# Optimization experiments

Hardware: AMD Instinct MI355X
Metric: run time of the kernel (lower is better)

The kernel has to match this reference:

```python
import jax, jax.numpy as jnp
import numpy as np
from jax import lax

B, H, W, C = 64, 224, 224, 3
FLAT = 27040  # 52*52*10 after localization convs/pools


def conv_relu(x, w, b):
    y = lax.conv_general_dilated(x, w, (1, 1), 'VALID',
                                 dimension_numbers=('NHWC', 'HWIO', 'NHWC'))
    return jax.nn.relu(y + b)


def maxpool2(x):
    return lax.reduce_window(x, -jnp.inf, lax.max, (1, 2, 2, 1), (1, 2, 2, 1), 'VALID')


def affine_grid(h, w, theta):
    # normalized coords in [-1, 1]
    xt, yt = jnp.meshgrid(jnp.linspace(-1.0, 1.0, w), jnp.linspace(-1.0, 1.0, h))
    grid = jnp.stack([xt.ravel(), yt.ravel(), jnp.ones(h * w, theta.dtype)], 0)  # (3, h*w)
    g = jnp.einsum('bij,jp->bip', theta, grid)  # (B, 2, h*w)
    return g.reshape(-1, 2, h, w)


def bilinear_sampler(img, xs, ys):
    # xs, ys: (B, h, w) in [-1, 1]; img: (B, H, W, C)
    max_y, max_x = img.shape[1] - 1, img.shape[2] - 1
    x = 0.5 * (xs + 1.0) * max_x
    y = 0.5 * (ys + 1.0) * max_y
    x0 = jnp.clip(jnp.floor(x).astype(jnp.int32), 0, max_x)
    x1 = jnp.clip(x0 + 1, 0, max_x)
    y0 = jnp.clip(jnp.floor(y).astype(jnp.int32), 0, max_y)
    y1 = jnp.clip(y0 + 1, 0, max_y)
    b = jnp.arange(img.shape[0])[:, None, None]
    Ia = img[b, y0, x0]  # (B,h,w,C)
    Ib = img[b, y1, x0]
    Ic = img[b, y0, x1]
    Id = img[b, y1, x1]
    x0f, x1f = x0.astype(x.dtype), x1.astype(x.dtype)
    y0f, y1f = y0.astype(y.dtype), y1.astype(y.dtype)
    wa = ((x1f - x) * (y1f - y))[..., None]
    wb = ((x1f - x) * (y - y0f))[..., None]
    wc = ((x - x0f) * (y1f - y))[..., None]
    wd = ((x - x0f) * (y - y0f))[..., None]
    return wa * Ia + wb * Ib + wc * Ic + wd * Id


def setup_inputs() -> dict:
    key = jax.random.key(0)
    ks = jax.random.split(key, 6)
    inputs = jax.random.normal(ks[0], (B, H, W, C), jnp.float32)
    conv1_w = jax.random.normal(ks[1], (7, 7, 3, 8), jnp.float32) * (2.0 / (7 * 7 * 3)) ** 0.5
    conv1_b = jnp.zeros((8,), jnp.float32)
    conv2_w = jax.random.normal(ks[2], (5, 5, 8, 10), jnp.float32) * (2.0 / (5 * 5 * 8)) ** 0.5
    conv2_b = jnp.zeros((10,), jnp.float32)
    fc1_w = jax.random.normal(ks[3], (FLAT, 32), jnp.float32) * (2.0 / FLAT) ** 0.5
    fc1_b = jnp.zeros((32,), jnp.float32)
    fc2_w = jax.random.normal(ks[4], (32, 6), jnp.float32) * 0.01
    fc2_b = jnp.array([1, 0, 0, 0, 1, 0], jnp.float32)  # identity affine init
    return dict(inputs=inputs, conv1_w=conv1_w, conv1_b=conv1_b,
                conv2_w=conv2_w, conv2_b=conv2_b, fc1_w=fc1_w, fc1_b=fc1_b,
                fc2_w=fc2_w, fc2_b=fc2_b)


def reference(inputs, conv1_w, conv1_b, conv2_w, conv2_b, fc1_w, fc1_b, fc2_w, fc2_b):
    xs = maxpool2(conv_relu(inputs, conv1_w, conv1_b))
    xs = maxpool2(conv_relu(xs, conv2_w, conv2_b))
    xs = xs.reshape(xs.shape[0], -1)  # (B, 27040)
    h1 = jax.nn.relu(xs @ fc1_w + fc1_b)
    theta = (h1 @ fc2_w + fc2_b).reshape(-1, 2, 3)
    grid = affine_grid(H, W, theta)  # (B, 2, H, W)
    return bilinear_sampler(inputs, grid[:, 0], grid[:, 1])
```

## Files before the change

kernel.cpp:

```cpp
#include <hip/hip_runtime.h>


__global__ __launch_bounds__(256) void k_wcvt(
    const float* __restrict__ w1, const float* __restrict__ b1,
    double* __restrict__ wd) {
  int t = blockIdx.x * 256 + threadIdx.x;
  if (t < 1176) wd[t] = (double)w1[t];
  else if (t < 1184) wd[t] = (double)b1[t - 1176];
}

__global__ __launch_bounds__(448) void k_conv1(
    const float* __restrict__ in, const double* __restrict__ wd,
    double* __restrict__ out) {
  __shared__ float win[14 * 672];

  int g = blockIdx.x & 7;
  int i = blockIdx.x >> 3;
  int b = g * 8 + i / 28;
  int tile = i % 28;
  int py0 = 4 * tile;
  int r0 = 8 * tile;

  {
    const float* ibb = in + (size_t)b * 150528;
    for (int idx = threadIdx.x; idx < 14 * 168; idx += 448) {
      int rr = idx / 168, c4 = idx % 168;
      int row = min(r0 + rr, 223);
      float4 v = reinterpret_cast<const float4*>(ibb + (size_t)row * 672)[c4];
      reinterpret_cast<float4*>(&win[rr * 672])[c4] = v;
    }
  }
  __syncthreads();

  int t = threadIdx.x;
  int py = py0 + t / 109;
  if (t < 436 && py < 109) {
    int px = t % 109;
    int lrb = 2 * (t / 109);

    double acc[2][2][8];
#pragma unroll
    for (int ii = 0; ii < 2; ++ii)
#pragma unroll
      for (int j = 0; j < 2; ++j)
#pragma unroll
        for (int k = 0; k < 8; ++k) acc[ii][j][k] = 0.0;

    for (int ky = 0; ky < 7; ++ky) {
      const float* r0p = &win[(lrb + ky) * 672 + 6 * px];
      const float* r1p = r0p + 672;
      float a0[24], a1[24];
#pragma unroll
      for (int j = 0; j < 12; ++j) {
        float2 u = reinterpret_cast<const float2*>(r0p)[j];
        a0[2 * j] = u.x; a0[2 * j + 1] = u.y;
        float2 v = reinterpret_cast<const float2*>(r1p)[j];
        a1[2 * j] = v.x; a1[2 * j + 1] = v.y;
      }
      const double* wk = wd + ky * 168;
#pragma unroll
      for (int kx = 0; kx < 7; ++kx) {
#pragma unroll
        for (int c = 0; c < 3; ++c) {
          double v00 = (double)a0[kx * 3 + c];
          double v01 = (double)a0[kx * 3 + 3 + c];
          double v10 = (double)a1[kx * 3 + c];
          double v11 = (double)a1[kx * 3 + 3 + c];
          const double* wp = wk + (kx * 3 + c) * 8;
#pragma unroll
          for (int oc = 0; oc < 8; ++oc) {
            double wv = wp[oc];
            acc[0][0][oc] = fma(v00, wv, acc[0][0][oc]);
            acc[0][1][oc] = fma(v01, wv, acc[0][1][oc]);
            acc[1][0][oc] = fma(v10, wv, acc[1][0][oc]);
            acc[1][1][oc] = fma(v11, wv, acc[1][1][oc]);
          }
        }
      }
    }

    double* op = out + ((size_t)b * 11881 + (size_t)py * 109 + px) * 8;
#pragma unroll
    for (int oc = 0; oc < 8; ++oc) {
      double m = fmax(fmax(acc[0][0][oc], acc[0][1][oc]),
                      fmax(acc[1][0][oc], acc[1][1][oc]));
      op[oc] = fmax(m + wd[1176 + oc], 0.0);
    }
  }
}

__global__ __launch_bounds__(448) void k_conv2(
    const double* __restrict__ in, const float* __restrict__ w,
    const float* __restrict__ bias, double* __restrict__ out) {
  __shared__ double win2[4 * 12 * 112];
  __shared__ double sw[200 * 12];
  __shared__ double sb[10];
  for (int i = threadIdx.x; i < 2000; i += 448) {
    int tap = i / 10, oc = i % 10;
    sw[tap * 12 + (oc / 5) * 6 + (oc % 5)] = (double)w[i];
  }
  if (threadIdx.x < 10) sb[threadIdx.x] = (double)bias[threadIdx.x];

  int g = blockIdx.x & 7;
  int i = blockIdx.x >> 3;
  int b = g * 8 + i / 13;
  int tile = i % 13;
  int py0 = 4 * tile;
  int r0 = 8 * tile;

  int t = threadIdx.x;
  bool valid = t < 416;
  int oh = t & 1;
  int p = t >> 1;
  int px = p % 52;
  int lrb = 2 * (p / 52);

  double acc[2][2][5];
#pragma unroll
  for (int ii = 0; ii < 2; ++ii)
#pragma unroll
    for (int jj = 0; jj < 2; ++jj)
#pragma unroll
      for (int k = 0; k < 5; ++k) acc[ii][jj][k] = 0.0;

  const double* ib = in + (size_t)b * 11881 * 8;

  for (int h = 0; h < 2; ++h) {
    __syncthreads();
    for (int idx = threadIdx.x; idx < 12 * 109 * 2; idx += 448) {
      int d2 = idx & 1;
      int x  = (idx >> 1) % 109;
      int rr = (idx >> 1) / 109;
      double2 v = *reinterpret_cast<const double2*>(
          ib + ((size_t)(r0 + rr) * 109 + x) * 8 + h * 4 + d2 * 2);
      win2[((d2 * 2) * 12 + rr) * 112 + x] = v.x;
      win2[((d2 * 2 + 1) * 12 + rr) * 112 + x] = v.y;
    }
    __syncthreads();

    if (valid) {
#pragma unroll
      for (int ky = 0; ky < 5; ++ky) {
        int rr0 = lrb + ky;
#pragma unroll
        for (int kx = 0; kx < 5; ++kx) {
          int xx = 2 * px + kx;
#pragma unroll
          for (int cc = 0; cc < 4; ++cc) {
            int c = h * 4 + cc;
            const double* pbase = &win2[(cc * 12 + rr0) * 112 + xx];
            double v00 = pbase[0];
            double v01 = pbase[1];
            double v10 = pbase[112];
            double v11 = pbase[113];
            const double* wp = &sw[((ky * 5 + kx) * 8 + c) * 12 + oh * 6];
#pragma unroll
            for (int oc = 0; oc < 5; ++oc) {
              double wv = wp[oc];
              acc[0][0][oc] = fma(v00, wv, acc[0][0][oc]);
              acc[0][1][oc] = fma(v01, wv, acc[0][1][oc]);
              acc[1][0][oc] = fma(v10, wv, acc[1][0][oc]);
              acc[1][1][oc] = fma(v11, wv, acc[1][1][oc]);
            }
          }
        }
      }
    }
  }

  if (valid) {
    int pix = py0 * 52 + p;
    double* op = out + ((size_t)b * 2704 + pix) * 10 + oh * 5;
#pragma unroll
    for (int oc = 0; oc < 5; ++oc) {
      double m = fmax(fmax(acc[0][0][oc], acc[0][1][oc]),
                      fmax(acc[1][0][oc], acc[1][1][oc]));
      op[oc] = fmax(m + sb[oh * 5 + oc], 0.0);
    }
  }
}

__global__ __launch_bounds__(256) void k_fc1(
    const double* __restrict__ xs, const float* __restrict__ w1,
    double* __restrict__ part) {
  int b = blockIdx.x >> 4;
  int q = blockIdx.x & 15;
  int oc = threadIdx.x & 31;
  int s = threadIdx.x >> 5;
  const double* xrow = xs + (size_t)b * 27040;

  int i0 = q * 1690 + s * 212;
  int i1 = min(i0 + 212, q * 1690 + 1690);
  double s0 = 0.0, s1 = 0.0;
  for (int i = i0; i + 1 < i1; i += 2) {
    s0 = fma(xrow[i],     (double)w1[(size_t)i * 32 + oc],       s0);
    s1 = fma(xrow[i + 1], (double)w1[(size_t)(i + 1) * 32 + oc], s1);
  }
  if ((i1 - i0) & 1)
    s0 = fma(xrow[i1 - 1], (double)w1[(size_t)(i1 - 1) * 32 + oc], s0);

  __shared__ double red[8][32];
  red[s][oc] = s0 + s1;
  __syncthreads();
  if (threadIdx.x < 32) {
    double v = 0.0;
#pragma unroll
    for (int k = 0; k < 8; ++k) v += red[k][threadIdx.x];
    part[((size_t)b * 16 + q) * 32 + threadIdx.x] = v;
  }
}

__global__ __launch_bounds__(64) void k_fc2(
    const double* __restrict__ part, const float* __restrict__ b1,
    const float* __restrict__ w2, const float* __restrict__ b2,
    double* __restrict__ theta) {
  int b = blockIdx.x;
  __shared__ double h1[32];
  if (threadIdx.x < 32) {
    double v = (double)b1[threadIdx.x];
#pragma unroll
    for (int q = 0; q < 16; ++q)
      v += part[((size_t)b * 16 + q) * 32 + threadIdx.x];
    h1[threadIdx.x] = v > 0.0 ? v : 0.0;
  }
  __syncthreads();
  if (threadIdx.x < 6) {
    double v = (double)b2[threadIdx.x];
#pragma unroll
    for (int k = 0; k < 32; ++k) v += h1[k] * (double)w2[k * 6 + threadIdx.x];
    theta[b * 6 + threadIdx.x] = v;
  }
}

__global__ __launch_bounds__(256) void k_sample(
    const float* __restrict__ img, const double* __restrict__ theta,
    float* __restrict__ out) {
  int idx = blockIdx.x * 256 + threadIdx.x;
  if (idx >= 64 * 224 * 224) return;
  int x = idx % 224;
  int t = idx / 224;
  int y = t % 224;
  int b = t / 224;

  const double* th = theta + b * 6;
  double t0 = th[0], t1 = th[1], t2 = th[2];
  double t3 = th[3], t4 = th[4], t5 = th[5];

  double xn = -1.0 + x * (2.0 / 223.0);
  double yn = -1.0 + y * (2.0 / 223.0);
  double xf = 0.5 * (t0 * xn + t1 * yn + t2 + 1.0) * 223.0;
  double yf = 0.5 * (t3 * xn + t4 * yn + t5 + 1.0) * 223.0;

  int x0 = (int)floor(xf);
  int y0 = (int)floor(yf);
  x0 = min(max(x0, 0), 223);
  y0 = min(max(y0, 0), 223);
  int x1 = min(x0 + 1, 223);
  int y1 = min(y0 + 1, 223);

  double x0f = (double)x0, x1f = (double)x1;
  double y0f = (double)y0, y1f = (double)y1;
  double wa = (x1f - xf) * (y1f - yf);
  double wb = (x1f - xf) * (yf - y0f);
  double wc = (xf - x0f) * (y1f - yf);
  double wd = (xf - x0f) * (yf - y0f);

  const float* p = img + (size_t)b * 150528;
  const float* Ia = p + ((size_t)y0 * 224 + x0) * 3;
  const float* Ib = p + ((size_t)y1 * 224 + x0) * 3;
  const float* Ic = p + ((size_t)y0 * 224 + x1) * 3;
  const float* Id = p + ((size_t)y1 * 224 + x1) * 3;

  float* op = out + (size_t)idx * 3;
#pragma unroll
  for (int c = 0; c < 3; ++c) {
    op[c] = (float)(wa * (double)Ia[c] + wb * (double)Ib[c] +
                    wc * (double)Ic[c] + wd * (double)Id[c]);
  }
}

extern "C" void kernel_launch(void* const* d_in, const int* in_sizes, int n_in,
                              void* d_out, int out_size, void* d_ws, size_t ws_size,
                              hipStream_t stream) {
  const float* inputs  = (const float*)d_in[0];
  const float* conv1_w = (const float*)d_in[1];
  const float* conv1_b = (const float*)d_in[2];
  const float* conv2_w = (const float*)d_in[3];
  const float* conv2_b = (const float*)d_in[4];
  const float* fc1_w   = (const float*)d_in[5];
  const float* fc1_b   = (const float*)d_in[6];
  const float* fc2_w   = (const float*)d_in[7];
  const float* fc2_b   = (const float*)d_in[8];
  float* outp = (float*)d_out;

  double* theta = (double*)d_ws;
  double* part  = (double*)((char*)d_ws + 4096);
  double* wd1   = (double*)((char*)d_ws + 4096 + 262144);
  double* pool1 = (double*)((char*)d_ws + 4096 + 262144 + 9472);
  double* pool2 = pool1 + 6083072;

  k_wcvt<<<5, 256, 0, stream>>>(conv1_w, conv1_b, wd1);
  k_conv1<<<28 * 64, 448, 0, stream>>>(inputs, wd1, pool1);
  k_conv2<<<13 * 64, 448, 0, stream>>>(pool1, conv2_w, conv2_b, pool2);
  k_fc1<<<1024, 256, 0, stream>>>(pool2, fc1_w, part);
  k_fc2<<<64, 64, 0, stream>>>(part, fc1_b, fc2_w, fc2_b, theta);
  k_sample<<<(64 * 224 * 224 + 255) / 256, 256, 0, stream>>>(inputs, theta, outp);
}
```

Baseline: 392.3 us.

## Restructure conv2: wave-uniform output half, even/odd LDS layout, global double weights

Conv2 weights and bias are now converted to double once in the weight-conversion kernel and read from global memory instead of being staged in LDS per block. Threads are regrouped so each half of the 512-thread block handles one group of five output channels (readfirstlane makes it wave-uniform), which lets weight reads become scalar loads. The LDS input window is split into even/odd column planes so the stride-2 pooled window is loaded once into registers and reused across kx taps. This cuts LDS traffic and per-block weight staging, but adds idle lanes (208 of 256 per half) and relies on scalar-cache weight loads.

```diff
diff --git a/kernel.cpp b/kernel.cpp
--- a/kernel.cpp
+++ b/kernel.cpp
@@ -3,10 +3,13 @@
 
 __global__ __launch_bounds__(256) void k_wcvt(
     const float* __restrict__ w1, const float* __restrict__ b1,
+    const float* __restrict__ w2, const float* __restrict__ b2,
     double* __restrict__ wd) {
   int t = blockIdx.x * 256 + threadIdx.x;
   if (t < 1176) wd[t] = (double)w1[t];
   else if (t < 1184) wd[t] = (double)b1[t - 1176];
+  else if (t < 3184) wd[t] = (double)w2[t - 1184];
+  else if (t < 3194) wd[t] = (double)b2[t - 3184];
 }
 
 __global__ __launch_bounds__(448) void k_conv1(
@@ -89,17 +92,10 @@
   }
 }
 
-__global__ __launch_bounds__(448) void k_conv2(
-    const double* __restrict__ in, const float* __restrict__ w,
-    const float* __restrict__ bias, double* __restrict__ out) {
-  __shared__ double win2[4 * 12 * 112];
-  __shared__ double sw[200 * 12];
-  __shared__ double sb[10];
-  for (int i = threadIdx.x; i < 2000; i += 448) {
-    int tap = i / 10, oc = i % 10;
-    sw[tap * 12 + (oc / 5) * 6 + (oc % 5)] = (double)w[i];
-  }
-  if (threadIdx.x < 10) sb[threadIdx.x] = (double)bias[threadIdx.x];
+__global__ __launch_bounds__(512) void k_conv2(
+    const double* __restrict__ in, const double* __restrict__ wd2,
+    double* __restrict__ out) {
+  __shared__ double win2[4 * 12 * 2 * 56];
 
   int g = blockIdx.x & 7;
   int i = blockIdx.x >> 3;
@@ -109,12 +105,14 @@
   int r0 = 8 * tile;
 
   int t = threadIdx.x;
-  bool valid = t < 416;
-  int oh = t & 1;
-  int p = t >> 1;
+  int oh = __builtin_amdgcn_readfirstlane(t >> 8);
+  int p = t & 255;
+  bool valid = p < 208;
   int px = p % 52;
   int lrb = 2 * (p / 52);
 
+  const double* wb = wd2 + oh * 5;
+
   double acc[2][2][5];
 #pragma unroll
   for (int ii = 0; ii < 2; ++ii)
@@ -127,14 +125,15 @@
 
   for (int h = 0; h < 2; ++h) {
     __syncthreads();
-    for (int idx = threadIdx.x; idx < 12 * 109 * 2; idx += 448) {
+    for (int idx = threadIdx.x; idx < 12 * 109 * 2; idx += 512) {
       int d2 = idx & 1;
       int x  = (idx >> 1) % 109;
       int rr = (idx >> 1) / 109;
       double2 v = *reinterpret_cast<const double2*>(
           ib + ((size_t)(r0 + rr) * 109 + x) * 8 + h * 4 + d2 * 2);
-      win2[((d2 * 2) * 12 + rr) * 112 + x] = v.x;
-      win2[((d2 * 2 + 1) * 12 + rr) * 112 + x] = v.y;
+      int par = x & 1, k = x >> 1;
+      win2[(((d2 * 2) * 12 + rr) * 2 + par) * 56 + k] = v.x;
+      win2[(((d2 * 2 + 1) * 12 + rr) * 2 + par) * 56 + k] = v.y;
     }
     __syncthreads();
 
@@ -143,17 +142,27 @@
       for (int ky = 0; ky < 5; ++ky) {
         int rr0 = lrb + ky;
 #pragma unroll
-        for (int kx = 0; kx < 5; ++kx) {
-          int xx = 2 * px + kx;
-#pragma unroll
-          for (int cc = 0; cc < 4; ++cc) {
-            int c = h * 4 + cc;
-            const double* pbase = &win2[(cc * 12 + rr0) * 112 + xx];
-            double v00 = pbase[0];
-            double v01 = pbase[1];
-            double v10 = pbase[112];
-            double v11 = pbase[113];
-            const double* wp = &sw[((ky * 5 + kx) * 8 + c) * 12 + oh * 6];
+        for (int cc = 0; cc < 4; ++cc) {
+          int c = h * 4 + cc;
+          const double* pe0 = &win2[((cc * 12 + rr0) * 2 + 0) * 56 + px];
+          const double* po0 = &win2[((cc * 12 + rr0) * 2 + 1) * 56 + px];
+          const double* pe1 = pe0 + 112;
+          const double* po1 = po0 + 112;
+          double e0[3] = {pe0[0], pe0[1], pe0[2]};
+          double o0[3] = {po0[0], po0[1], po0[2]};
+          double e1[3] = {pe1[0], pe1[1], pe1[2]};
+          double o1[3] = {po1[0], po1[1], po1[2]};
+#pragma unroll
+          for (int kx = 0; kx < 5; ++kx) {
+            double v00, v01, v10, v11;
+            if (kx & 1) {
+              v00 = o0[kx >> 1]; v01 = e0[(kx >> 1) + 1];
+              v10 = o1[kx >> 1]; v11 = e1[(kx >> 1) + 1];
+            } else {
+              v00 = e0[kx >> 1]; v01 = o0[kx >> 1];
+              v10 = e1[kx >> 1]; v11 = o1[kx >> 1];
+            }
+            const double* wp = wb + ((ky * 5 + kx) * 8 + c) * 10;
 #pragma unroll
             for (int oc = 0; oc < 5; ++oc) {
               double wv = wp[oc];
@@ -175,7 +184,7 @@
     for (int oc = 0; oc < 5; ++oc) {
       double m = fmax(fmax(acc[0][0][oc], acc[0][1][oc]),
                       fmax(acc[1][0][oc], acc[1][1][oc]));
-      op[oc] = fmax(m + sb[oh * 5 + oc], 0.0);
+      op[oc] = fmax(m + wd2[2000 + oh * 5 + oc], 0.0);
     }
   }
 }
@@ -295,13 +304,13 @@
 
   double* theta = (double*)d_ws;
   double* part  = (double*)((char*)d_ws + 4096);
-  double* wd1   = (double*)((char*)d_ws + 4096 + 262144);
-  double* pool1 = (double*)((char*)d_ws + 4096 + 262144 + 9472);
+  double* wd    = (double*)((char*)d_ws + 4096 + 262144);
+  double* pool1 = (double*)((char*)d_ws + 4096 + 262144 + 25600);
   double* pool2 = pool1 + 6083072;
 
-  k_wcvt<<<5, 256, 0, stream>>>(conv1_w, conv1_b, wd1);
-  k_conv1<<<28 * 64, 448, 0, stream>>>(inputs, wd1, pool1);
-  k_conv2<<<13 * 64, 448, 0, stream>>>(pool1, conv2_w, conv2_b, pool2);
+  k_wcvt<<<13, 256, 0, stream>>>(conv1_w, conv1_b, conv2_w, conv2_b, wd);
+  k_conv1<<<28 * 64, 448, 0, stream>>>(inputs, wd, pool1);
+  k_conv2<<<13 * 64, 512, 0, stream>>>(pool1, wd + 1184, pool2);
   k_fc1<<<1024, 256, 0, stream>>>(pool2, fc1_w, part);
   k_fc2<<<64, 64, 0, stream>>>(part, fc1_b, fc2_w, fc2_b, theta);
   k_sample<<<(64 * 224 * 224 + 255) / 256, 256, 0, stream>>>(inputs, theta, outp);
```

After: 394.3 us. Within noise of the previous version (+0.5%).
